# Performance work log

Hardware: AMD Instinct MI355X
Metric: run time of the kernel (lower is better)

The kernel has to match this reference:

```python
import jax, jax.numpy as jnp
import numpy as np

N_NODES = 100000
N_EDGES = 1600000
N_GRAPHS = 1000
X_S = 128
HID = 64


def setup_inputs() -> dict:
    key = jax.random.key(0)
    ks = jax.random.split(key, 12)
    x = jax.random.normal(ks[0], (N_NODES, X_S), dtype=jnp.float32)
    edge_index = jax.random.randint(ks[1], (2, N_EDGES), 0, N_NODES, dtype=jnp.int64)
    batch = jnp.sort(jax.random.randint(ks[2], (N_NODES,), 0, N_GRAPHS, dtype=jnp.int64))
    def lin(k, fin, fout):
        s = 1.0 / np.sqrt(fin)
        kw, kb = jax.random.split(k)
        W = jax.random.uniform(kw, (fin, fout), minval=-s, maxval=s, dtype=jnp.float32)
        b = jax.random.uniform(kb, (fout,), minval=-s, maxval=s, dtype=jnp.float32)
        return W, b
    W1, b1 = lin(ks[3], X_S, HID)
    W2, b2 = lin(ks[4], HID, HID)
    W3, b3 = lin(ks[5], HID, HID)
    Wf, bf = lin(ks[6], HID, 10)
    Wl, bl = lin(ks[7], 10, 1)
    eps1 = jnp.float32(0.37)
    eps2 = jnp.float32(0.72)
    eps3 = jnp.float32(0.11)
    return {"x": x, "edge_index": edge_index, "batch": batch,
            "W1": W1, "b1": b1, "W2": W2, "b2": b2, "W3": W3, "b3": b3,
            "Wf": Wf, "bf": bf, "Wl": Wl, "bl": bl,
            "eps1": eps1, "eps2": eps2, "eps3": eps3}


def _gin_conv(h, src, dst, eps, W, b):
    # GIN: nn((1+eps)*x_i + sum_{j in N(i)} x_j); messages flow src -> dst
    agg = jax.ops.segment_sum(h[src], dst, num_segments=N_NODES)  # [N, d]
    return ((1.0 + eps) * h + agg) @ W + b


def reference(x, edge_index, batch, W1, b1, W2, b2, W3, b3, Wf, bf, Wl, bl,
              eps1, eps2, eps3):
    src, dst = edge_index[0], edge_index[1]
    h = jax.nn.relu(_gin_conv(x, src, dst, eps1, W1, b1))
    h = jax.nn.relu(_gin_conv(h, src, dst, eps2, W2, b2))
    h = jax.nn.relu(_gin_conv(h, src, dst, eps3, W3, b3))
    # global_mean_pool over graph ids
    sums = jax.ops.segment_sum(h, batch, num_segments=N_GRAPHS)        # [G, 64]
    cnts = jax.ops.segment_sum(jnp.ones((N_NODES,), h.dtype), batch,
                               num_segments=N_GRAPHS)                   # [G]
    pooled = sums / jnp.maximum(cnts, 1.0)[:, None]
    out = jax.nn.relu(pooled @ Wf + bf) @ Wl + bl                       # [G, 1]
    return out
```

## Files before the change

### kernel.cpp

```cpp
#include <hip/hip_runtime.h>

#define N_NODES 100000
#define N_EDGES 1600000
#define N_GRAPHS 1000

#define NB_C 391
#define B1   256
#define CHUNK (N_EDGES / B1)
#define MTOT (NB_C * B1)

typedef unsigned int uint32;
typedef unsigned short ushort16;
typedef __attribute__((ext_vector_type(8))) short short8;
typedef __attribute__((ext_vector_type(4))) float f32x4;

static __device__ __forceinline__ ushort16 f2bf(float f) {
    uint32 u = __float_as_uint(f);
    u += 0x7fffu + ((u >> 16) & 1u);
    return (ushort16)(u >> 16);
}
static __device__ __forceinline__ uint32 pk2(float a, float b) {
    return (uint32)f2bf(a) | ((uint32)f2bf(b) << 16);
}
static __device__ __forceinline__ void bf2x(uint32 v, float& lo, float& hi) {
    lo = __uint_as_float(v << 16);
    hi = __uint_as_float(v & 0xffff0000u);
}
static __device__ __forceinline__ void acc8(float* a, uint4 v) {
    float lo, hi;
    bf2x(v.x, lo, hi); a[0] += lo; a[1] += hi;
    bf2x(v.y, lo, hi); a[2] += lo; a[3] += hi;
    bf2x(v.z, lo, hi); a[4] += lo; a[5] += hi;
    bf2x(v.w, lo, hi); a[6] += lo; a[7] += hi;
}

union CV8 { uint4 u; short8 s; };

__global__ __launch_bounds__(256) void convw_kernel(
    const float* __restrict__ W1, const float* __restrict__ W2,
    const float* __restrict__ W3,
    ushort16* __restrict__ W1t, ushort16* __restrict__ W2t,
    ushort16* __restrict__ W3t)
{
    int t = threadIdx.x;
    if (blockIdx.x == 0) {
        for (int i = t; i < 64 * 128; i += 256) {
            int j = i >> 7, k = i & 127;
            W1t[i] = f2bf(W1[k * 64 + j]);
        }
    } else if (blockIdx.x == 1) {
        for (int i = t; i < 64 * 64; i += 256) {
            int j = i >> 6, k = i & 63;
            W2t[i] = f2bf(W2[k * 64 + j]);
        }
    } else {
        for (int i = t; i < 64 * 64; i += 256) {
            int j = i >> 6, k = i & 63;
            W3t[i] = f2bf(W3[k * 64 + j]);
        }
    }
}


__global__ __launch_bounds__(256) void count_kernel(
    const int* __restrict__ dst, int* __restrict__ M)
{
    __shared__ int cnt[NB_C];
    int b = blockIdx.x, t = threadIdx.x;
    for (int q = t; q < NB_C; q += 256) cnt[q] = 0;
    __syncthreads();
    int e0 = b * CHUNK;
    for (int e = e0 + t; e < e0 + CHUNK; e += 256)
        atomicAdd(&cnt[dst[e] >> 8], 1);
    __syncthreads();
    for (int q = t; q < NB_C; q += 256) M[q * B1 + b] = cnt[q];
}

#define SCAN_B 1024
#define SCAN_NBLK ((MTOT + SCAN_B - 1) / SCAN_B)

__global__ __launch_bounds__(256) void scanA_kernel(
    const int* __restrict__ in, int* __restrict__ excl, int* __restrict__ bsum)
{
    __shared__ int s[256];
    int b = blockIdx.x, t = threadIdx.x;
    int base = b * SCAN_B + t * 4;
    int v[4];
#pragma unroll
    for (int i = 0; i < 4; ++i) v[i] = (base + i < MTOT) ? in[base + i] : 0;
    int tsum = v[0] + v[1] + v[2] + v[3];
    s[t] = tsum;
    __syncthreads();
    for (int off = 1; off < 256; off <<= 1) {
        int x = (t >= off) ? s[t - off] : 0;
        __syncthreads();
        s[t] += x;
        __syncthreads();
    }
    int run = s[t] - tsum;
#pragma unroll
    for (int i = 0; i < 4; ++i) {
        if (base + i < MTOT) excl[base + i] = run;
        run += v[i];
    }
    if (t == 255) bsum[b] = s[255];
}

__global__ __launch_bounds__(256) void scanB_kernel(int* __restrict__ bsum)
{
    __shared__ int s[256];
    int t = threadIdx.x;
    int v = (t < SCAN_NBLK) ? bsum[t] : 0;
    s[t] = v;
    __syncthreads();
    for (int off = 1; off < 256; off <<= 1) {
        int x = (t >= off) ? s[t - off] : 0;
        __syncthreads();
        s[t] += x;
        __syncthreads();
    }
    if (t < SCAN_NBLK) bsum[t] = s[t] - v;
}

__global__ __launch_bounds__(256) void scanC_kernel(
    const int* __restrict__ excl, const int* __restrict__ bsum,
    int* __restrict__ out)
{
    int b = blockIdx.x, t = threadIdx.x;
    int add = bsum[b];
    int base = b * SCAN_B + t * 4;
#pragma unroll
    for (int i = 0; i < 4; ++i)
        if (base + i < MTOT) out[base + i] = excl[base + i] + add;
}

__global__ __launch_bounds__(256) void scatter_kernel(
    const int* __restrict__ src, const int* __restrict__ dst,
    const int* __restrict__ Ms, uint32* __restrict__ tmp)
{
    __shared__ int cnt[NB_C];
    __shared__ int loc[NB_C + 1];
    __shared__ int cur[NB_C];
    __shared__ uint32 staged[CHUNK];
    int b = blockIdx.x, t = threadIdx.x;
    int e0 = b * CHUNK;

    for (int q = t; q < NB_C; q += 256) cnt[q] = 0;
    __syncthreads();
    for (int e = e0 + t; e < e0 + CHUNK; e += 256)
        atomicAdd(&cnt[dst[e] >> 8], 1);
    __syncthreads();
    if (t == 0) {
        int r = 0;
        for (int q = 0; q < NB_C; ++q) { loc[q] = r; r += cnt[q]; }
        loc[NB_C] = r;
    }
    __syncthreads();
    for (int q = t; q < NB_C; q += 256) cur[q] = loc[q];
    __syncthreads();
    for (int e = e0 + t; e < e0 + CHUNK; e += 256) {
        int d = dst[e];
        int q = d >> 8;
        int pos = atomicAdd(&cur[q], 1);
        staged[pos] = ((uint32)(d & 255) << 17) | (uint32)src[e];
    }
    __syncthreads();
    for (int i = t; i < CHUNK; i += 256) {
        int lo = 0, hi = NB_C - 1;
        while (lo < hi) {
            int mid = (lo + hi + 1) >> 1;
            if (loc[mid] <= i) lo = mid; else hi = mid - 1;
        }
        int gpos = Ms[lo * B1 + b] + (i - loc[lo]);
        tmp[gpos] = staged[i];
    }
}

__global__ __launch_bounds__(256) void finalize_kernel(
    const uint32* __restrict__ tmp, const int* __restrict__ Ms,
    int* __restrict__ row_off, int* __restrict__ esrc)
{
    __shared__ int cnt[256];
    __shared__ int pref[256];
    __shared__ int cur[256];
    int q = blockIdx.x, t = threadIdx.x;
    int start = Ms[q * B1];
    int end = (q == NB_C - 1) ? N_EDGES : Ms[(q + 1) * B1];

    cnt[t] = 0;
    __syncthreads();
    for (int e = start + t; e < end; e += 256)
        atomicAdd(&cnt[tmp[e] >> 17], 1);
    __syncthreads();
    pref[t] = cnt[t];
    __syncthreads();
    for (int off = 1; off < 256; off <<= 1) {
        int x = (t >= off) ? pref[t - off] : 0;
        __syncthreads();
        pref[t] += x;
        __syncthreads();
    }
    {
        int excl = pref[t] - cnt[t];
        int node = q * 256 + t;
        if (node < N_NODES) row_off[node] = start + excl;
        cur[t] = start + excl;
    }
    if (q == 0 && t == 0) row_off[N_NODES] = N_EDGES;
    __syncthreads();
    for (int e = start + t; e < end; e += 256) {
        uint32 u = tmp[e];
        int pos = atomicAdd(&cur[u >> 17], 1);
        esrc[pos] = (int)(u & 0x1FFFFu);
    }
}

__global__ __launch_bounds__(256) void gemm1_mfma_kernel(
    const float* __restrict__ x,
    const ushort16* __restrict__ Wt,
    ushort16* __restrict__ y)
{
    int lane = threadIdx.x & 63;
    int wave = threadIdx.x >> 6;
    int col = lane & 15, quad = lane >> 4;
    int node0 = blockIdx.x * 64 + wave * 16;
    int anode = node0 + col;

    short8 a[4];
    if (anode < N_NODES) {
        const float* xr = &x[(size_t)anode * 128 + quad * 8];
#pragma unroll
        for (int s = 0; s < 4; ++s) {
            float4 v0 = *(const float4*)&xr[s * 32];
            float4 v1 = *(const float4*)&xr[s * 32 + 4];
            CV8 cv;
            cv.u = make_uint4(pk2(v0.x, v0.y), pk2(v0.z, v0.w),
                              pk2(v1.x, v1.y), pk2(v1.z, v1.w));
            a[s] = cv.s;
        }
    } else {
        short8 z = {0, 0, 0, 0, 0, 0, 0, 0};
#pragma unroll
        for (int s = 0; s < 4; ++s) a[s] = z;
    }

    f32x4 acc[4];
#pragma unroll
    for (int nt = 0; nt < 4; ++nt)
#pragma unroll
        for (int r = 0; r < 4; ++r) acc[nt][r] = 0.0f;

#pragma unroll
    for (int nt = 0; nt < 4; ++nt) {
        const ushort16* wr = &Wt[(size_t)(nt * 16 + col) * 128 + quad * 8];
#pragma unroll
        for (int s = 0; s < 4; ++s) {
            short8 b = *(const short8*)&wr[s * 32];
            acc[nt] = __builtin_amdgcn_mfma_f32_16x16x32_bf16(a[s], b, acc[nt], 0, 0, 0);
        }
    }

#pragma unroll
    for (int nt = 0; nt < 4; ++nt)
#pragma unroll
        for (int r = 0; r < 4; ++r) {
            int node = node0 + quad * 4 + r;
            if (node < N_NODES)
                y[(size_t)node * 64 + nt * 16 + col] = f2bf(acc[nt][r]);
        }
}

__global__ __launch_bounds__(256) void aggregate_kernel(
    const uint4* __restrict__ y4,
    const int* __restrict__ row_off,
    const int* __restrict__ esrc,
    const float* __restrict__ b,
    const float* __restrict__ eps_p,
    uint4* __restrict__ out4)
{
    int lane = threadIdx.x & 63;
    int wave = threadIdx.x >> 6;
    int grp = lane >> 3;
    int w = lane & 7;
    int node = blockIdx.x * 32 + wave * 8 + grp;

    int s0 = row_off[node], s1 = row_off[node + 1];
    float a[8], c[8];
#pragma unroll
    for (int i = 0; i < 8; ++i) { a[i] = 0.f; c[i] = 0.f; }

    int e = s0;
    for (; e + 3 < s1; e += 4) {
        int i0 = esrc[e];
        int i1 = esrc[e + 1];
        int i2 = esrc[e + 2];
        int i3 = esrc[e + 3];
        uint4 v0 = y4[(size_t)i0 * 8 + w];
        uint4 v1 = y4[(size_t)i1 * 8 + w];
        uint4 v2 = y4[(size_t)i2 * 8 + w];
        uint4 v3 = y4[(size_t)i3 * 8 + w];
        acc8(a, v0);
        acc8(c, v1);
        acc8(a, v2);
        acc8(c, v3);
    }
    for (; e < s1; ++e) {
        uint4 v0 = y4[(size_t)esrc[e] * 8 + w];
        acc8(a, v0);
    }
#pragma unroll
    for (int i = 0; i < 8; ++i) a[i] += c[i];

    uint4 sv = y4[(size_t)node * 8 + w];
    float s[8];
    bf2x(sv.x, s[0], s[1]);
    bf2x(sv.y, s[2], s[3]);
    bf2x(sv.z, s[4], s[5]);
    bf2x(sv.w, s[6], s[7]);
    float ep1 = 1.0f + eps_p[0];
    float4 b0 = *(const float4*)&b[w * 8];
    float4 b1 = *(const float4*)&b[w * 8 + 4];
    float r0 = fmaxf(fmaf(ep1, s[0], a[0]) + b0.x, 0.0f);
    float r1 = fmaxf(fmaf(ep1, s[1], a[1]) + b0.y, 0.0f);
    float r2 = fmaxf(fmaf(ep1, s[2], a[2]) + b0.z, 0.0f);
    float r3 = fmaxf(fmaf(ep1, s[3], a[3]) + b0.w, 0.0f);
    float r4 = fmaxf(fmaf(ep1, s[4], a[4]) + b1.x, 0.0f);
    float r5 = fmaxf(fmaf(ep1, s[5], a[5]) + b1.y, 0.0f);
    float r6 = fmaxf(fmaf(ep1, s[6], a[6]) + b1.z, 0.0f);
    float r7 = fmaxf(fmaf(ep1, s[7], a[7]) + b1.w, 0.0f);
    out4[(size_t)node * 8 + w] =
        make_uint4(pk2(r0, r1), pk2(r2, r3), pk2(r4, r5), pk2(r6, r7));
}

__global__ __launch_bounds__(256) void agg_gemm_fused_kernel(
    const uint4* __restrict__ h4,
    const int* __restrict__ row_off,
    const int* __restrict__ esrc,
    const ushort16* __restrict__ Wt,
    const float* __restrict__ bias,
    const float* __restrict__ eps_p,
    ushort16* __restrict__ hout)
{
    __shared__ __align__(16) ushort16 zl[4][16][72];
    int lane = threadIdx.x & 63;
    int wave = threadIdx.x >> 6;
    int g = lane >> 2;
    int c = lane & 3;
    int node0 = blockIdx.x * 64 + wave * 16;
    if (node0 >= N_NODES) return;
    int node = node0 + g;

    int s0 = row_off[node], s1 = row_off[node + 1];
    float a[16], d[16];
#pragma unroll
    for (int i = 0; i < 16; ++i) { a[i] = 0.f; d[i] = 0.f; }

    const size_t cb = (size_t)c * 2;
    int e = s0;
    for (; e + 3 < s1; e += 4) {
        int i0 = esrc[e];
        int i1 = esrc[e + 1];
        int i2 = esrc[e + 2];
        int i3 = esrc[e + 3];
        uint4 v0a = h4[(size_t)i0 * 8 + cb], v0b = h4[(size_t)i0 * 8 + cb + 1];
        uint4 v1a = h4[(size_t)i1 * 8 + cb], v1b = h4[(size_t)i1 * 8 + cb + 1];
        uint4 v2a = h4[(size_t)i2 * 8 + cb], v2b = h4[(size_t)i2 * 8 + cb + 1];
        uint4 v3a = h4[(size_t)i3 * 8 + cb], v3b = h4[(size_t)i3 * 8 + cb + 1];
        acc8(a, v0a); acc8(a + 8, v0b);
        acc8(d, v1a); acc8(d + 8, v1b);
        acc8(a, v2a); acc8(a + 8, v2b);
        acc8(d, v3a); acc8(d + 8, v3b);
    }
    for (; e < s1; ++e) {
        int i0 = esrc[e];
        uint4 va = h4[(size_t)i0 * 8 + cb], vb = h4[(size_t)i0 * 8 + cb + 1];
        acc8(a, va); acc8(a + 8, vb);
    }
#pragma unroll
    for (int i = 0; i < 16; ++i) a[i] += d[i];

    uint4 sva = h4[(size_t)node * 8 + cb], svb = h4[(size_t)node * 8 + cb + 1];
    float s[16];
    bf2x(sva.x, s[0], s[1]);  bf2x(sva.y, s[2], s[3]);
    bf2x(sva.z, s[4], s[5]);  bf2x(sva.w, s[6], s[7]);
    bf2x(svb.x, s[8], s[9]);  bf2x(svb.y, s[10], s[11]);
    bf2x(svb.z, s[12], s[13]); bf2x(svb.w, s[14], s[15]);
    float ep1 = 1.0f + eps_p[0];
    float z[16];
#pragma unroll
    for (int i = 0; i < 16; ++i) z[i] = fmaf(ep1, s[i], a[i]);

    uint4 pA = make_uint4(pk2(z[0], z[1]), pk2(z[2], z[3]),
                          pk2(z[4], z[5]), pk2(z[6], z[7]));
    uint4 pB = make_uint4(pk2(z[8], z[9]), pk2(z[10], z[11]),
                          pk2(z[12], z[13]), pk2(z[14], z[15]));
    *(uint4*)&zl[wave][g][c * 16] = pA;
    *(uint4*)&zl[wave][g][c * 16 + 8] = pB;

    int col = lane & 15, quad = lane >> 4;
    short8 a0 = *(const short8*)&zl[wave][col][quad * 8];
    short8 a1 = *(const short8*)&zl[wave][col][32 + quad * 8];

    f32x4 acc[4];
#pragma unroll
    for (int nt = 0; nt < 4; ++nt)
#pragma unroll
        for (int r = 0; r < 4; ++r) acc[nt][r] = 0.0f;

#pragma unroll
    for (int nt = 0; nt < 4; ++nt) {
        const ushort16* wr = &Wt[(size_t)(nt * 16 + col) * 64 + quad * 8];
        short8 b0 = *(const short8*)&wr[0];
        short8 b1 = *(const short8*)&wr[32];
        acc[nt] = __builtin_amdgcn_mfma_f32_16x16x32_bf16(a0, b0, acc[nt], 0, 0, 0);
        acc[nt] = __builtin_amdgcn_mfma_f32_16x16x32_bf16(a1, b1, acc[nt], 0, 0, 0);
    }

#pragma unroll
    for (int nt = 0; nt < 4; ++nt) {
        float bl = bias[nt * 16 + col];
#pragma unroll
        for (int r = 0; r < 4; ++r) {
            int nd = node0 + quad * 4 + r;
            hout[(size_t)nd * 64 + nt * 16 + col] =
                f2bf(fmaxf(acc[nt][r] + bl, 0.0f));
        }
    }
}

__global__ __launch_bounds__(256) void pool_head_kernel(
    const uint32* __restrict__ hb,
    const int* __restrict__ batch,
    const float* __restrict__ Wf,
    const float* __restrict__ bfv,
    const float* __restrict__ Wl,
    const float* __restrict__ blv,
    float* __restrict__ out)
{
    __shared__ float red[4][64];
    __shared__ float pooled[64];
    __shared__ float hid[10];
    int g = blockIdx.x;
    int t = threadIdx.x;
    int lo = 0, hi = N_NODES;
    while (lo < hi) { int mid = (lo + hi) >> 1; if (batch[mid] < g) lo = mid + 1; else hi = mid; }
    int start = lo;
    hi = N_NODES;
    while (lo < hi) { int mid = (lo + hi) >> 1; if (batch[mid] < g + 1) lo = mid + 1; else hi = mid; }
    int end = lo;

    int c = t & 63, nl = t >> 6;
    int wd = c >> 1, odd = c & 1;
    float acc = 0.0f;
    for (int i = start + nl; i < end; i += 4) {
        uint32 u = hb[(size_t)i * 32 + wd];
        acc += __uint_as_float(odd ? (u & 0xffff0000u) : (u << 16));
    }
    red[nl][c] = acc;
    __syncthreads();
    if (t < 64) {
        float cnt = (float)(end - start);
        float inv = 1.0f / fmaxf(cnt, 1.0f);
        pooled[t] = (red[0][t] + red[1][t] + red[2][t] + red[3][t]) * inv;
    }
    __syncthreads();
    if (t < 10) {
        float s = bfv[t];
#pragma unroll
        for (int k = 0; k < 64; ++k) s = fmaf(pooled[k], Wf[k * 10 + t], s);
        hid[t] = fmaxf(s, 0.0f);
    }
    __syncthreads();
    if (t == 0) {
        float s = blv[0];
#pragma unroll
        for (int j = 0; j < 10; ++j) s = fmaf(hid[j], Wl[j], s);
        out[g] = s;
    }
}

extern "C" void kernel_launch(void* const* d_in, const int* in_sizes, int n_in,
                              void* d_out, int out_size, void* d_ws, size_t ws_size,
                              hipStream_t stream)
{
    const float* x     = (const float*)d_in[0];
    const int*   ei    = (const int*)  d_in[1];
    const int*   src   = ei;
    const int*   dst   = ei + N_EDGES;
    const int*   batch = (const int*)  d_in[2];
    const float* W1    = (const float*)d_in[3];
    const float* b1    = (const float*)d_in[4];
    const float* W2    = (const float*)d_in[5];
    const float* b2    = (const float*)d_in[6];
    const float* W3    = (const float*)d_in[7];
    const float* b3    = (const float*)d_in[8];
    const float* Wf    = (const float*)d_in[9];
    const float* bfv   = (const float*)d_in[10];
    const float* Wl    = (const float*)d_in[11];
    const float* blv   = (const float*)d_in[12];
    const float* eps1  = (const float*)d_in[13];
    const float* eps2  = (const float*)d_in[14];
    const float* eps3  = (const float*)d_in[15];

    ushort16* ybA = (ushort16*)d_ws;
    ushort16* ybB = ybA + (size_t)N_NODES * 64;
    int*   ints = (int*)(ybB + (size_t)N_NODES * 64);
    int*   M       = ints;
    int*   Mex     = M + MTOT;
    int*   Ms      = Mex + MTOT;
    int*   bsum    = Ms + MTOT;
    int*   row_off = bsum + 256;
    int*   esrc    = row_off + N_NODES + 1;
    uint32* tmp    = (uint32*)(esrc + N_EDGES);
    ushort16* W1t = (ushort16*)(((uintptr_t)(tmp + N_EDGES) + 255) & ~(uintptr_t)255);
    ushort16* W2t = W1t + 64 * 128;
    ushort16* W3t = W2t + 64 * 64;

    const int gemm_blk  = (N_NODES + 63) / 64;
    const int agg_blk   = N_NODES / 32;
    const int fused_blk = (N_NODES + 63) / 64;

    convw_kernel<<<3, 256, 0, stream>>>(W1, W2, W3, W1t, W2t, W3t);

    count_kernel<<<B1, 256, 0, stream>>>(dst, M);
    scanA_kernel<<<SCAN_NBLK, 256, 0, stream>>>(M, Mex, bsum);
    scanB_kernel<<<1, 256, 0, stream>>>(bsum);
    scanC_kernel<<<SCAN_NBLK, 256, 0, stream>>>(Mex, bsum, Ms);
    scatter_kernel<<<B1, 256, 0, stream>>>(src, dst, Ms, tmp);
    finalize_kernel<<<NB_C, 256, 0, stream>>>(tmp, Ms, row_off, esrc);

    gemm1_mfma_kernel<<<gemm_blk, 256, 0, stream>>>(x, W1t, ybA);
    aggregate_kernel<<<agg_blk, 256, 0, stream>>>(
        (const uint4*)ybA, row_off, esrc, b1, eps1, (uint4*)ybB);

    agg_gemm_fused_kernel<<<fused_blk, 256, 0, stream>>>(
        (const uint4*)ybB, row_off, esrc, W2t, b2, eps2, ybA);

    agg_gemm_fused_kernel<<<fused_blk, 256, 0, stream>>>(
        (const uint4*)ybA, row_off, esrc, W3t, b3, eps3, ybB);

    pool_head_kernel<<<N_GRAPHS, 256, 0, stream>>>(
        (const uint32*)ybB, batch, Wf, bfv, Wl, blv, (float*)d_out);
}
```

Measured before the change: 333.4 us.

## Increase CSR-build chunk count and stage scatter/finalize writes in shared memory

```diff
diff --git a/kernel.cpp b/kernel.cpp
--- a/kernel.cpp
+++ b/kernel.cpp
@@ -5,9 +5,10 @@
 #define N_GRAPHS 1000
 
 #define NB_C 391
-#define B1   256
-#define CHUNK (N_EDGES / B1)
+#define B1   1024
+#define CHUNK_E ((N_EDGES + B1 - 1) / B1)
 #define MTOT (NB_C * B1)
+#define STG_MAX 4736
 
 typedef unsigned int uint32;
 typedef unsigned short ushort16;
@@ -69,15 +70,16 @@
     int b = blockIdx.x, t = threadIdx.x;
     for (int q = t; q < NB_C; q += 256) cnt[q] = 0;
     __syncthreads();
-    int e0 = b * CHUNK;
-    for (int e = e0 + t; e < e0 + CHUNK; e += 256)
+    int e0 = b * CHUNK_E;
+    int e1 = e0 + CHUNK_E; if (e1 > N_EDGES) e1 = N_EDGES;
+    for (int e = e0 + t; e < e1; e += 256)
         atomicAdd(&cnt[dst[e] >> 8], 1);
     __syncthreads();
     for (int q = t; q < NB_C; q += 256) M[q * B1 + b] = cnt[q];
 }
 
 #define SCAN_B 1024
-#define SCAN_NBLK ((MTOT + SCAN_B - 1) / SCAN_B)
+#define SCAN_NBLK (MTOT / SCAN_B)
 
 __global__ __launch_bounds__(256) void scanA_kernel(
     const int* __restrict__ in, int* __restrict__ excl, int* __restrict__ bsum)
@@ -106,14 +108,14 @@
     if (t == 255) bsum[b] = s[255];
 }
 
-__global__ __launch_bounds__(256) void scanB_kernel(int* __restrict__ bsum)
-{
-    __shared__ int s[256];
+__global__ __launch_bounds__(512) void scanB_kernel(int* __restrict__ bsum)
+{
+    __shared__ int s[512];
     int t = threadIdx.x;
     int v = (t < SCAN_NBLK) ? bsum[t] : 0;
     s[t] = v;
     __syncthreads();
-    for (int off = 1; off < 256; off <<= 1) {
+    for (int off = 1; off < 512; off <<= 1) {
         int x = (t >= off) ? s[t - off] : 0;
         __syncthreads();
         s[t] += x;
@@ -139,40 +141,52 @@
     const int* __restrict__ Ms, uint32* __restrict__ tmp)
 {
     __shared__ int cnt[NB_C];
-    __shared__ int loc[NB_C + 1];
+    __shared__ int loc[NB_C];
     __shared__ int cur[NB_C];
-    __shared__ uint32 staged[CHUNK];
+    __shared__ int msb[NB_C];
+    __shared__ int ssum[256];
+    __shared__ uint32 staged[CHUNK_E];
+    __shared__ unsigned short bkt[CHUNK_E];
     int b = blockIdx.x, t = threadIdx.x;
-    int e0 = b * CHUNK;
-
-    for (int q = t; q < NB_C; q += 256) cnt[q] = 0;
-    __syncthreads();
-    for (int e = e0 + t; e < e0 + CHUNK; e += 256)
+    int e0 = b * CHUNK_E;
+    int e1 = e0 + CHUNK_E; if (e1 > N_EDGES) e1 = N_EDGES;
+    int n = e1 - e0;
+
+    for (int q = t; q < NB_C; q += 256) {
+        cnt[q] = 0;
+        msb[q] = Ms[q * B1 + b];
+    }
+    __syncthreads();
+    for (int e = e0 + t; e < e1; e += 256)
         atomicAdd(&cnt[dst[e] >> 8], 1);
     __syncthreads();
-    if (t == 0) {
-        int r = 0;
-        for (int q = 0; q < NB_C; ++q) { loc[q] = r; r += cnt[q]; }
-        loc[NB_C] = r;
-    }
-    __syncthreads();
-    for (int q = t; q < NB_C; q += 256) cur[q] = loc[q];
-    __syncthreads();
-    for (int e = e0 + t; e < e0 + CHUNK; e += 256) {
+    int q0 = 2 * t, q1 = 2 * t + 1;
+    int c0 = (q0 < NB_C) ? cnt[q0] : 0;
+    int c1 = (q1 < NB_C) ? cnt[q1] : 0;
+    int pairsum = c0 + c1;
+    ssum[t] = pairsum;
+    __syncthreads();
+    for (int off = 1; off < 256; off <<= 1) {
+        int x = (t >= off) ? ssum[t - off] : 0;
+        __syncthreads();
+        ssum[t] += x;
+        __syncthreads();
+    }
+    int excl = ssum[t] - pairsum;
+    if (q0 < NB_C) { loc[q0] = excl; cur[q0] = excl; }
+    if (q1 < NB_C) { loc[q1] = excl + c0; cur[q1] = excl + c0; }
+    __syncthreads();
+    for (int e = e0 + t; e < e1; e += 256) {
         int d = dst[e];
         int q = d >> 8;
         int pos = atomicAdd(&cur[q], 1);
         staged[pos] = ((uint32)(d & 255) << 17) | (uint32)src[e];
-    }
-    __syncthreads();
-    for (int i = t; i < CHUNK; i += 256) {
-        int lo = 0, hi = NB_C - 1;
-        while (lo < hi) {
-            int mid = (lo + hi + 1) >> 1;
-            if (loc[mid] <= i) lo = mid; else hi = mid - 1;
-        }
-        int gpos = Ms[lo * B1 + b] + (i - loc[lo]);
-        tmp[gpos] = staged[i];
+        bkt[pos] = (unsigned short)q;
+    }
+    __syncthreads();
+    for (int i = t; i < n; i += 256) {
+        int q = bkt[i];
+        tmp[msb[q] + (i - loc[q])] = staged[i];
     }
 }
 
@@ -183,9 +197,11 @@
     __shared__ int cnt[256];
     __shared__ int pref[256];
     __shared__ int cur[256];
+    __shared__ uint32 stg[STG_MAX];
     int q = blockIdx.x, t = threadIdx.x;
     int start = Ms[q * B1];
     int end = (q == NB_C - 1) ? N_EDGES : Ms[(q + 1) * B1];
+    int seg = end - start;
 
     cnt[t] = 0;
     __syncthreads();
@@ -204,14 +220,25 @@
         int excl = pref[t] - cnt[t];
         int node = q * 256 + t;
         if (node < N_NODES) row_off[node] = start + excl;
-        cur[t] = start + excl;
+        cur[t] = excl;
     }
     if (q == 0 && t == 0) row_off[N_NODES] = N_EDGES;
     __syncthreads();
-    for (int e = start + t; e < end; e += 256) {
-        uint32 u = tmp[e];
-        int pos = atomicAdd(&cur[u >> 17], 1);
-        esrc[pos] = (int)(u & 0x1FFFFu);
+    if (seg <= STG_MAX) {
+        for (int e = start + t; e < end; e += 256) {
+            uint32 u = tmp[e];
+            int pos = atomicAdd(&cur[u >> 17], 1);
+            stg[pos] = u & 0x1FFFFu;
+        }
+        __syncthreads();
+        for (int i = t; i < seg; i += 256)
+            esrc[start + i] = (int)stg[i];
+    } else {
+        for (int e = start + t; e < end; e += 256) {
+            uint32 u = tmp[e];
+            int pos = atomicAdd(&cur[u >> 17], 1);
+            esrc[start + pos] = (int)(u & 0x1FFFFu);
+        }
     }
 }
 
@@ -509,7 +536,7 @@
     int*   Mex     = M + MTOT;
     int*   Ms      = Mex + MTOT;
     int*   bsum    = Ms + MTOT;
-    int*   row_off = bsum + 256;
+    int*   row_off = bsum + 512;
     int*   esrc    = row_off + N_NODES + 1;
     uint32* tmp    = (uint32*)(esrc + N_EDGES);
     ushort16* W1t = (ushort16*)(((uintptr_t)(tmp + N_EDGES) + 255) & ~(uintptr_t)255);
@@ -524,7 +551,7 @@
 
     count_kernel<<<B1, 256, 0, stream>>>(dst, M);
     scanA_kernel<<<SCAN_NBLK, 256, 0, stream>>>(M, Mex, bsum);
-    scanB_kernel<<<1, 256, 0, stream>>>(bsum);
+    scanB_kernel<<<1, 512, 0, stream>>>(bsum);
     scanC_kernel<<<SCAN_NBLK, 256, 0, stream>>>(Mex, bsum, Ms);
     scatter_kernel<<<B1, 256, 0, stream>>>(src, dst, Ms, tmp);
     finalize_kernel<<<NB_C, 256, 0, stream>>>(tmp, Ms, row_off, esrc);
```

Result: faster. 304.7 us (-8.6%).
